# Kernel tuning notes

Hardware: AMD Instinct MI355X
Metric: run time of the kernel (lower is better)

The kernel has to match this reference:

```python
import jax, jax.numpy as jnp
import numpy as np

N = 100_000      # num_nodes
E = 1_600_000    # num_edges (avg degree 16)
D = 64           # embedding_dim
L = 3            # num_layers


def setup_inputs() -> dict:
    key = jax.random.key(0)
    k1, k2 = jax.random.split(key)
    edge_index = jax.random.randint(k1, (2, E), 0, N, dtype=jnp.int64)
    edge_weight = jnp.ones((E,), jnp.float32)
    # nn.init.normal_(std=0.1)
    embedding = 0.1 * jax.random.normal(k2, (N, D), dtype=jnp.float32)
    return {"embedding": embedding, "edge_weight": edge_weight, "edge_index": edge_index}


def reference(embedding, edge_weight, edge_index):
    n = embedding.shape[0]
    self_idx = jnp.arange(n, dtype=edge_index.dtype)
    # add_self_loops: append (i, i) with weight 1 (PyG default fill_value)
    row = jnp.concatenate([edge_index[0], self_idx])  # source j
    col = jnp.concatenate([edge_index[1], self_idx])  # target i
    ew = jnp.concatenate([edge_weight, jnp.ones((n,), embedding.dtype)])
    # degree() counts occurrences of row (unweighted)
    deg = jax.ops.segment_sum(jnp.ones_like(ew), row, num_segments=n)
    deg_inv_sqrt = jnp.where(deg > 0, jax.lax.rsqrt(deg), 0.0)
    norm = deg_inv_sqrt[row] * ew * deg_inv_sqrt[col]  # [E+N]

    x = embedding
    acc = embedding  # running sum of layer-0..L embeddings
    for _ in range(L):
        # gather from source, scale, scatter-add to target (dropout off in eval)
        msg = norm[:, None] * x[row]                       # [E+N, D]
        x = jax.ops.segment_sum(msg, col, num_segments=n)  # [N, D]
        acc = acc + x
    return acc / (L + 1)
```

## Files before the change

kernel.cpp:

```cpp
#include <hip/hip_runtime.h>
#include <stdint.h>

#define DIM 64
#define GB 128
#define GSH 7
#define CH 2048
#define TB1 256
#define BINS2 50000
#define RANGES 2
#define NSLICE 64
#define TBH 1024

__device__ __forceinline__ unsigned bf16rne(float f) {
    unsigned u = __float_as_uint(f);
    return (u + 0x7FFFu + ((u >> 16) & 1u)) >> 16;
}
__device__ __forceinline__ unsigned pack2(float lo, float hi) {
    return bf16rne(lo) | (bf16rne(hi) << 16);
}
#define UNPK(u, lo, hi) { lo = __uint_as_float((u) << 16); hi = __uint_as_float((u) & 0xFFFF0000u); }

__global__ void __launch_bounds__(TBH)
hist_src_kernel(const int* __restrict__ src, const int* __restrict__ dst,
                unsigned short* __restrict__ partials, int* __restrict__ bcnt,
                int E, int N, int Es, int NB) {
    __shared__ unsigned h32[BINS2 / 2];
    __shared__ int hb[1024];
    const int b = blockIdx.x;
    const int r = b / NSLICE, s = b % NSLICE;
    const int base = r * BINS2;
    const int hi = min(base + BINS2, N);
    const int nbw = (hi - base + 1) >> 1;
    for (int j = threadIdx.x; j < nbw; j += TBH) h32[j] = 0;
    if (r == 0) for (int j = threadIdx.x; j < NB; j += TBH) hb[j] = 0;
    __syncthreads();
    const int e0 = s * Es, e1 = min(e0 + Es, E);
    if (r == 0) {
#pragma unroll 4
        for (int i = e0 + threadIdx.x; i < e1; i += TBH) {
            unsigned j = (unsigned)(src[i] - base);
            if (j < (unsigned)BINS2) atomicAdd(&h32[j >> 1], 1u << ((j & 1) * 16));
            atomicAdd(&hb[((unsigned)dst[i]) >> GSH], 1);
        }
    } else {
#pragma unroll 4
        for (int i = e0 + threadIdx.x; i < e1; i += TBH) {
            unsigned j = (unsigned)(src[i] - base);
            if (j < (unsigned)BINS2) atomicAdd(&h32[j >> 1], 1u << ((j & 1) * 16));
        }
    }
    __syncthreads();
    unsigned* part = (unsigned*)(partials + (size_t)s * N + base);
    for (int j = threadIdx.x; j < nbw; j += TBH) part[j] = h32[j];
    if (r == 0)
        for (int j = threadIdx.x; j < NB; j += TBH)
            if (hb[j]) atomicAdd(&bcnt[j], hb[j]);
}

__global__ void __launch_bounds__(256)
merge_dis_kernel(const unsigned short* __restrict__ partials, float* __restrict__ dis, int N) {
    const int i = blockIdx.x * blockDim.x + threadIdx.x;
    if (i >= N) return;
    int od = 0;
    for (int s = 0; s < NSLICE; ++s) od += partials[(size_t)s * N + i];
    dis[i] = rsqrtf((float)od + 1.0f);
}

__global__ void scan_buckets(const int* __restrict__ bcnt, int* __restrict__ bucket_base,
                             int* __restrict__ cursor, int* __restrict__ offsets,
                             int NB, int N) {
    __shared__ int buf[1024];
    const int t = threadIdx.x;
    int v = (t < NB) ? bcnt[t] : 0;
    buf[t] = v;
    __syncthreads();
    for (int off = 1; off < 1024; off <<= 1) {
        int add = (t >= off) ? buf[t - off] : 0;
        __syncthreads();
        buf[t] += add;
        __syncthreads();
    }
    if (t < NB) { bucket_base[t] = buf[t] - v; cursor[t] = buf[t] - v; }
    if (t == NB - 1) { bucket_base[NB] = buf[t]; offsets[N] = buf[t]; }
}

__global__ void __launch_bounds__(TB1)
part_kernel(const int* __restrict__ src, const int* __restrict__ dst,
            const float* __restrict__ ew,
            int* __restrict__ cursor, int2* __restrict__ staged, int E, int NB) {
    __shared__ int h[1024];
    const int tid = threadIdx.x;
    const int e0 = blockIdx.x * CH;
    const int e1 = min(e0 + CH, E);
    for (int j = tid; j < NB; j += TB1) h[j] = 0;
    __syncthreads();
    int4 d[CH / (TB1 * 4)];
    int ngrp = 0;
    for (int i = e0 + tid * 4, k = 0; i < e1; i += TB1 * 4, ++k) {
        int4 t;
        if (i + 3 < e1) t = *(const int4*)(dst + i);
        else {
            t.x = dst[i];
            t.y = (i + 1 < e1) ? dst[i + 1] : -1;
            t.z = (i + 2 < e1) ? dst[i + 2] : -1;
            t.w = (i + 3 < e1) ? dst[i + 3] : -1;
        }
        d[k] = t;
        if (t.x >= 0) atomicAdd(&h[t.x >> GSH], 1);
        if (t.y >= 0) atomicAdd(&h[t.y >> GSH], 1);
        if (t.z >= 0) atomicAdd(&h[t.z >> GSH], 1);
        if (t.w >= 0) atomicAdd(&h[t.w >> GSH], 1);
        ngrp = k + 1;
    }
    __syncthreads();
    for (int j = tid; j < NB; j += TB1) {
        int c = h[j];
        h[j] = c ? atomicAdd(&cursor[j], c) : 0;
    }
    __syncthreads();
    for (int i = e0 + tid * 4, k = 0; k < ngrp; i += TB1 * 4, ++k) {
        int4 t = d[k];
        int4 ss = make_int4(0, 0, 0, 0);
        float4 ww = make_float4(0.f, 0.f, 0.f, 0.f);
        if (i + 3 < e1) { ss = *(const int4*)(src + i); ww = *(const float4*)(ew + i); }
        else {
            ss.x = src[i]; ww.x = ew[i];
            if (i + 1 < e1) { ss.y = src[i + 1]; ww.y = ew[i + 1]; }
            if (i + 2 < e1) { ss.z = src[i + 2]; ww.z = ew[i + 2]; }
            if (i + 3 < e1) { ss.w = src[i + 3]; ww.w = ew[i + 3]; }
        }
#define PART1(T, S, W) if ((T) >= 0) { \
        int pos_ = atomicAdd(&h[(T) >> GSH], 1); \
        staged[pos_] = make_int2((S) | (((T) & (GB - 1)) << 20), __float_as_int(W)); }
        PART1(t.x, ss.x, ww.x)
        PART1(t.y, ss.y, ww.y)
        PART1(t.z, ss.z, ww.z)
        PART1(t.w, ss.w, ww.w)
#undef PART1
    }
}

__global__ void __launch_bounds__(256)
place_kernel(const int2* __restrict__ staged, const int* __restrict__ bucket_base,
             const float* __restrict__ dis,
             int* __restrict__ offsets, int2* __restrict__ csr, int N) {
    __shared__ int cnt[GB];
    __shared__ int cur[GB];
    __shared__ int pre[GB + 1];
    __shared__ float disb[GB];
    const int b = blockIdx.x;
    const int n0 = b << GSH;
    const int nb = min(GB, N - n0);
    const int r0 = bucket_base[b], r1 = bucket_base[b + 1];
    for (int j = threadIdx.x; j < GB; j += 256) cnt[j] = 0;
    for (int j = threadIdx.x; j < nb; j += 256) disb[j] = dis[n0 + j];
    __syncthreads();
    for (int i = r0 + threadIdx.x; i < r1; i += 256)
        atomicAdd(&cnt[(staged[i].x >> 20) & (GB - 1)], 1);
    __syncthreads();
    if (threadIdx.x == 0) {
        int run = r0;
        for (int j = 0; j < nb; ++j) { pre[j] = run; run += cnt[j]; }
        pre[nb] = run;
    }
    __syncthreads();
    for (int j = threadIdx.x; j < nb; j += 256) { offsets[n0 + j] = pre[j]; cur[j] = pre[j]; }
    __syncthreads();
    for (int i = r0 + threadIdx.x; i < r1; i += 256) {
        int2 rec = staged[i];
        int tl = (rec.x >> 20) & (GB - 1);
        int s = rec.x & 0xFFFFF;
        int rank = atomicAdd(&cur[tl], 1);
        float w = dis[s] * __int_as_float(rec.y) * disb[tl];
        csr[rank] = make_int2(s, __float_as_int(w));
    }
}

__global__ void __launch_bounds__(256)
conv_kernel(const float4* __restrict__ in4, uint4* __restrict__ outb, int n8) {
    int i = blockIdx.x * blockDim.x + threadIdx.x;
    if (i >= n8) return;
    float4 a = in4[2 * i], b = in4[2 * i + 1];
    uint4 o;
    o.x = pack2(a.x, a.y); o.y = pack2(a.z, a.w);
    o.z = pack2(b.x, b.y); o.w = pack2(b.z, b.w);
    outb[i] = o;
}

__global__ void __launch_bounds__(256)
prop_kernel(const uint4* __restrict__ xg, const float4* __restrict__ selfF,
            uint4* __restrict__ xstore,
            const int* __restrict__ offsets, const int2* __restrict__ csr,
            const float* __restrict__ dis, int n,
            const float4* __restrict__ embF, const uint4* __restrict__ xaF,
            float4* __restrict__ outF) {
    const int lane = threadIdx.x & 63;
    const int fl  = lane & 7;
    const int sub = lane >> 3;
    const int wave = blockIdx.x * (blockDim.x >> 6) + (threadIdx.x >> 6);
    const int node = wave * 8 + sub;
    if (node >= n) return;

    const int beg = offsets[node];
    const int end = offsets[node + 1];
    const float d = dis[node];
    const float dd = d * d;

    float a0, a1, a2, a3, a4, a5, a6, a7;
    uint4 qs = make_uint4(0, 0, 0, 0);
    if (selfF) {
        float4 s0 = selfF[(size_t)node * 16 + fl * 2];
        float4 s1 = selfF[(size_t)node * 16 + fl * 2 + 1];
        a0 = dd * s0.x; a1 = dd * s0.y; a2 = dd * s0.z; a3 = dd * s0.w;
        a4 = dd * s1.x; a5 = dd * s1.y; a6 = dd * s1.z; a7 = dd * s1.w;
    } else {
        qs = xg[(size_t)node * 8 + fl];
        float l, h;
        UNPK(qs.x, l, h) a0 = dd * l; a1 = dd * h;
        UNPK(qs.y, l, h) a2 = dd * l; a3 = dd * h;
        UNPK(qs.z, l, h) a4 = dd * l; a5 = dd * h;
        UNPK(qs.w, l, h) a6 = dd * l; a7 = dd * h;
    }

#define EDGE(E, Q) { float w_ = __int_as_float((E).y); float l, h; \
    UNPK((Q).x, l, h) a0 = fmaf(w_, l, a0); a1 = fmaf(w_, h, a1); \
    UNPK((Q).y, l, h) a2 = fmaf(w_, l, a2); a3 = fmaf(w_, h, a3); \
    UNPK((Q).z, l, h) a4 = fmaf(w_, l, a4); a5 = fmaf(w_, h, a5); \
    UNPK((Q).w, l, h) a6 = fmaf(w_, l, a6); a7 = fmaf(w_, h, a7); }

    int p = beg;
    for (; p + 8 <= end; p += 8) {
        int2 e0 = csr[p + 0], e1 = csr[p + 1], e2 = csr[p + 2], e3 = csr[p + 3];
        int2 e4 = csr[p + 4], e5 = csr[p + 5], e6 = csr[p + 6], e7 = csr[p + 7];
        uint4 q0 = xg[(size_t)e0.x * 8 + fl];
        uint4 q1 = xg[(size_t)e1.x * 8 + fl];
        uint4 q2 = xg[(size_t)e2.x * 8 + fl];
        uint4 q3 = xg[(size_t)e3.x * 8 + fl];
        uint4 q4 = xg[(size_t)e4.x * 8 + fl];
        uint4 q5 = xg[(size_t)e5.x * 8 + fl];
        uint4 q6 = xg[(size_t)e6.x * 8 + fl];
        uint4 q7 = xg[(size_t)e7.x * 8 + fl];
        EDGE(e0, q0) EDGE(e1, q1) EDGE(e2, q2) EDGE(e3, q3)
        EDGE(e4, q4) EDGE(e5, q5) EDGE(e6, q6) EDGE(e7, q7)
    }
    for (; p + 4 <= end; p += 4) {
        int2 e0 = csr[p + 0], e1 = csr[p + 1], e2 = csr[p + 2], e3 = csr[p + 3];
        uint4 q0 = xg[(size_t)e0.x * 8 + fl];
        uint4 q1 = xg[(size_t)e1.x * 8 + fl];
        uint4 q2 = xg[(size_t)e2.x * 8 + fl];
        uint4 q3 = xg[(size_t)e3.x * 8 + fl];
        EDGE(e0, q0) EDGE(e1, q1) EDGE(e2, q2) EDGE(e3, q3)
    }
    for (; p < end; ++p) {
        int2 e = csr[p];
        uint4 q = xg[(size_t)e.x * 8 + fl];
        EDGE(e, q)
    }
#undef EDGE

    if (outF) {
        float4 eA = embF[(size_t)node * 16 + fl * 2];
        float4 eB = embF[(size_t)node * 16 + fl * 2 + 1];
        uint4 qa = xaF[(size_t)node * 8 + fl];
        float r0 = eA.x + a0, r1 = eA.y + a1, r2 = eA.z + a2, r3 = eA.w + a3;
        float r4 = eB.x + a4, r5 = eB.y + a5, r6 = eB.z + a6, r7 = eB.w + a7;
        float l, h;
        UNPK(qa.x, l, h) r0 += l; r1 += h;
        UNPK(qa.y, l, h) r2 += l; r3 += h;
        UNPK(qa.z, l, h) r4 += l; r5 += h;
        UNPK(qa.w, l, h) r6 += l; r7 += h;
        UNPK(qs.x, l, h) r0 += l; r1 += h;
        UNPK(qs.y, l, h) r2 += l; r3 += h;
        UNPK(qs.z, l, h) r4 += l; r5 += h;
        UNPK(qs.w, l, h) r6 += l; r7 += h;
        outF[(size_t)node * 16 + fl * 2] =
            make_float4(0.25f * r0, 0.25f * r1, 0.25f * r2, 0.25f * r3);
        outF[(size_t)node * 16 + fl * 2 + 1] =
            make_float4(0.25f * r4, 0.25f * r5, 0.25f * r6, 0.25f * r7);
    } else {
        uint4 o;
        o.x = pack2(a0, a1); o.y = pack2(a2, a3);
        o.z = pack2(a4, a5); o.w = pack2(a6, a7);
        xstore[(size_t)node * 8 + fl] = o;
    }
}


extern "C" void kernel_launch(void* const* d_in, const int* in_sizes, int n_in,
                              void* d_out, int out_size, void* d_ws, size_t ws_size,
                              hipStream_t stream) {
    const float* emb = (const float*)d_in[0];
    const float* ew  = (const float*)d_in[1];
    const int*   ei  = (const int*)d_in[2];
    const int E = in_sizes[2] / 2;
    const int N = in_sizes[0] / DIM;
    const int* src = ei;
    const int* dst = ei + E;
    float* out = (float*)d_out;

    const int NB = (N + GB - 1) >> GSH;
    const int Es = (E + NSLICE - 1) / NSLICE;

    char* w = (char*)d_ws;
    size_t xSz = ((size_t)N * DIM * 2 + 255) & ~(size_t)255;
    size_t sSz = ((size_t)E * 8 + 255) & ~(size_t)255;
    size_t pSz = ((size_t)NSLICE * N * 2 + 255) & ~(size_t)255;
    size_t uSz = xSz > sSz ? xSz : sSz; if (pSz > uSz) uSz = pSz;
    unsigned short* partials = (unsigned short*)w;
    int2* staged = (int2*)w;
    uint4* xb    = (uint4*)w; w += uSz;
    int2* csr    = (int2*)w; w += sSz;
    uint4* x0c   = (uint4*)w; w += xSz;
    uint4* xa    = (uint4*)w; w += xSz;
    int* offsets = (int*)w; w += ((size_t)(N + 1) * 4 + 255) & ~(size_t)255;
    float* dis   = (float*)w; w += ((size_t)N * 4 + 255) & ~(size_t)255;
    int* bcnt        = (int*)w; w += 1024 * 4;
    int* bucket_base = (int*)w; w += 1025 * 4;
    int* cursor      = (int*)w; w += 1024 * 4;

    const int TB = 256;
    hipMemsetAsync(bcnt, 0, (size_t)NB * 4, stream);

    hist_src_kernel<<<RANGES * NSLICE, TBH, 0, stream>>>(src, dst, partials, bcnt,
                                                         E, N, Es, NB);
    merge_dis_kernel<<<(N + TB - 1) / TB, TB, 0, stream>>>(partials, dis, N);
    scan_buckets<<<1, 1024, 0, stream>>>(bcnt, bucket_base, cursor, offsets, NB, N);
    part_kernel<<<(E + CH - 1) / CH, TB1, 0, stream>>>(src, dst, ew, cursor,
                                                       staged, E, NB);
    place_kernel<<<NB, TB, 0, stream>>>(staged, bucket_base, dis, offsets, csr, N);

    const int n8 = N * DIM / 8;
    conv_kernel<<<(n8 + TB - 1) / TB, TB, 0, stream>>>((const float4*)emb, x0c, n8);

    dim3 grid((N + 31) / 32), block(TB);
    prop_kernel<<<grid, block, 0, stream>>>(x0c, (const float4*)emb, xa,
                                            offsets, csr, dis, N,
                                            nullptr, nullptr, nullptr);
    prop_kernel<<<grid, block, 0, stream>>>(xa, nullptr, xb,
                                            offsets, csr, dis, N,
                                            nullptr, nullptr, nullptr);
    prop_kernel<<<grid, block, 0, stream>>>(xb, nullptr, nullptr,
                                            offsets, csr, dis, N,
                                            (const float4*)emb, xa, (float4*)out);
}
```

Baseline: 284.0 us.

## Restructure CSR build: 8-bit full-range histograms, fused merge/scan and part/conv

```diff
diff --git a/kernel.cpp b/kernel.cpp
--- a/kernel.cpp
+++ b/kernel.cpp
@@ -2,13 +2,12 @@
 #include <stdint.h>
 
 #define DIM 64
-#define GB 128
-#define GSH 7
+#define GB 256
+#define GSH 8
 #define CH 2048
 #define TB1 256
-#define BINS2 50000
-#define RANGES 2
-#define NSLICE 64
+#define HW 25000
+#define NSL 256
 #define TBH 1024
 
 __device__ __forceinline__ unsigned bf16rne(float f) {
@@ -21,78 +20,96 @@
 #define UNPK(u, lo, hi) { lo = __uint_as_float((u) << 16); hi = __uint_as_float((u) & 0xFFFF0000u); }
 
 __global__ void __launch_bounds__(TBH)
-hist_src_kernel(const int* __restrict__ src, const int* __restrict__ dst,
-                unsigned short* __restrict__ partials, int* __restrict__ bcnt,
-                int E, int N, int Es, int NB) {
-    __shared__ unsigned h32[BINS2 / 2];
-    __shared__ int hb[1024];
-    const int b = blockIdx.x;
-    const int r = b / NSLICE, s = b % NSLICE;
-    const int base = r * BINS2;
-    const int hi = min(base + BINS2, N);
-    const int nbw = (hi - base + 1) >> 1;
-    for (int j = threadIdx.x; j < nbw; j += TBH) h32[j] = 0;
-    if (r == 0) for (int j = threadIdx.x; j < NB; j += TBH) hb[j] = 0;
+hist_kernel(const int* __restrict__ src, const int* __restrict__ dst,
+            unsigned* __restrict__ partials, int* __restrict__ bslice,
+            int E, int N, int Es, int NB) {
+    __shared__ unsigned h8[HW];
+    __shared__ int hb[512];
+    const int s = blockIdx.x;
+    const int nw = (N + 3) >> 2;
+    for (int j = threadIdx.x; j < nw; j += TBH) h8[j] = 0;
+    for (int j = threadIdx.x; j < 512; j += TBH) hb[j] = 0;
     __syncthreads();
     const int e0 = s * Es, e1 = min(e0 + Es, E);
-    if (r == 0) {
 #pragma unroll 4
-        for (int i = e0 + threadIdx.x; i < e1; i += TBH) {
-            unsigned j = (unsigned)(src[i] - base);
-            if (j < (unsigned)BINS2) atomicAdd(&h32[j >> 1], 1u << ((j & 1) * 16));
-            atomicAdd(&hb[((unsigned)dst[i]) >> GSH], 1);
+    for (int i = e0 + threadIdx.x; i < e1; i += TBH) {
+        unsigned sj = (unsigned)src[i];
+        unsigned tj = (unsigned)dst[i];
+        atomicAdd(&h8[sj >> 2], 1u << ((sj & 3) * 8));
+        atomicAdd(&hb[tj >> GSH], 1);
+    }
+    __syncthreads();
+    unsigned* part = partials + (size_t)s * nw;
+    for (int j = threadIdx.x; j < nw; j += TBH) part[j] = h8[j];
+    for (int j = threadIdx.x; j < NB; j += TBH) bslice[s * 512 + j] = hb[j];
+}
+
+__global__ void __launch_bounds__(512)
+merge_scan_kernel(const unsigned* __restrict__ partials, const int* __restrict__ bslice,
+                  float* __restrict__ dis, int* __restrict__ bucket_base,
+                  int* __restrict__ cursor, int* __restrict__ offsets,
+                  int nw, int nmerge, int N, int NB) {
+    __shared__ int buf[512];
+    if ((int)blockIdx.x < nmerge) {
+        const int w = blockIdx.x * 512 + threadIdx.x;
+        if (w >= nw) return;
+        int s0 = 0, s1 = 0, s2 = 0, s3 = 0;
+#pragma unroll 8
+        for (int s = 0; s < NSL; ++s) {
+            unsigned v = partials[(size_t)s * nw + w];
+            s0 += v & 255u; s1 += (v >> 8) & 255u;
+            s2 += (v >> 16) & 255u; s3 += v >> 24;
+        }
+        const int nidx = w * 4;
+        if (nidx + 3 < N) {
+            *(float4*)(dis + nidx) = make_float4(
+                rsqrtf((float)s0 + 1.f), rsqrtf((float)s1 + 1.f),
+                rsqrtf((float)s2 + 1.f), rsqrtf((float)s3 + 1.f));
+        } else {
+            if (nidx + 0 < N) dis[nidx + 0] = rsqrtf((float)s0 + 1.f);
+            if (nidx + 1 < N) dis[nidx + 1] = rsqrtf((float)s1 + 1.f);
+            if (nidx + 2 < N) dis[nidx + 2] = rsqrtf((float)s2 + 1.f);
+            if (nidx + 3 < N) dis[nidx + 3] = rsqrtf((float)s3 + 1.f);
         }
     } else {
-#pragma unroll 4
-        for (int i = e0 + threadIdx.x; i < e1; i += TBH) {
-            unsigned j = (unsigned)(src[i] - base);
-            if (j < (unsigned)BINS2) atomicAdd(&h32[j >> 1], 1u << ((j & 1) * 16));
-        }
-    }
-    __syncthreads();
-    unsigned* part = (unsigned*)(partials + (size_t)s * N + base);
-    for (int j = threadIdx.x; j < nbw; j += TBH) part[j] = h32[j];
-    if (r == 0)
-        for (int j = threadIdx.x; j < NB; j += TBH)
-            if (hb[j]) atomicAdd(&bcnt[j], hb[j]);
-}
-
-__global__ void __launch_bounds__(256)
-merge_dis_kernel(const unsigned short* __restrict__ partials, float* __restrict__ dis, int N) {
-    const int i = blockIdx.x * blockDim.x + threadIdx.x;
-    if (i >= N) return;
-    int od = 0;
-    for (int s = 0; s < NSLICE; ++s) od += partials[(size_t)s * N + i];
-    dis[i] = rsqrtf((float)od + 1.0f);
-}
-
-__global__ void scan_buckets(const int* __restrict__ bcnt, int* __restrict__ bucket_base,
-                             int* __restrict__ cursor, int* __restrict__ offsets,
-                             int NB, int N) {
-    __shared__ int buf[1024];
-    const int t = threadIdx.x;
-    int v = (t < NB) ? bcnt[t] : 0;
-    buf[t] = v;
-    __syncthreads();
-    for (int off = 1; off < 1024; off <<= 1) {
-        int add = (t >= off) ? buf[t - off] : 0;
+        const int t = threadIdx.x;
+        int v = 0;
+        if (t < NB)
+            for (int s = 0; s < NSL; ++s) v += bslice[s * 512 + t];
+        buf[t] = v;
         __syncthreads();
-        buf[t] += add;
-        __syncthreads();
-    }
-    if (t < NB) { bucket_base[t] = buf[t] - v; cursor[t] = buf[t] - v; }
-    if (t == NB - 1) { bucket_base[NB] = buf[t]; offsets[N] = buf[t]; }
+        for (int off = 1; off < 512; off <<= 1) {
+            int add = (t >= off) ? buf[t - off] : 0;
+            __syncthreads();
+            buf[t] += add;
+            __syncthreads();
+        }
+        if (t < NB) { bucket_base[t] = buf[t] - v; cursor[t] = buf[t] - v; }
+        if (t == NB - 1) { bucket_base[NB] = buf[t]; offsets[N] = buf[t]; }
+    }
 }
 
 __global__ void __launch_bounds__(TB1)
-part_kernel(const int* __restrict__ src, const int* __restrict__ dst,
-            const float* __restrict__ ew,
-            int* __restrict__ cursor, int2* __restrict__ staged, int E, int NB) {
-    __shared__ int h[1024];
+part_conv_kernel(const int* __restrict__ src, const int* __restrict__ dst,
+                 const float* __restrict__ ew,
+                 int* __restrict__ cursor, int2* __restrict__ staged,
+                 const float4* __restrict__ emb4, uint4* __restrict__ x0c,
+                 int E, int NB, int npart, int n8) {
+    __shared__ int h[512];
+    if ((int)blockIdx.x >= npart) {
+        const int i = (blockIdx.x - npart) * TB1 + threadIdx.x;
+        if (i >= n8) return;
+        float4 a = emb4[2 * i], b = emb4[2 * i + 1];
+        uint4 o;
+        o.x = pack2(a.x, a.y); o.y = pack2(a.z, a.w);
+        o.z = pack2(b.x, b.y); o.w = pack2(b.z, b.w);
+        x0c[i] = o;
+        return;
+    }
     const int tid = threadIdx.x;
     const int e0 = blockIdx.x * CH;
     const int e1 = min(e0 + CH, E);
-    for (int j = tid; j < NB; j += TB1) h[j] = 0;
+    for (int j = tid; j < 512; j += TB1) h[j] = 0;
     __syncthreads();
     int4 d[CH / (TB1 * 4)];
     int ngrp = 0;
@@ -152,8 +169,8 @@
     const int n0 = b << GSH;
     const int nb = min(GB, N - n0);
     const int r0 = bucket_base[b], r1 = bucket_base[b + 1];
-    for (int j = threadIdx.x; j < GB; j += 256) cnt[j] = 0;
-    for (int j = threadIdx.x; j < nb; j += 256) disb[j] = dis[n0 + j];
+    cnt[threadIdx.x] = 0;
+    disb[threadIdx.x] = (threadIdx.x < nb) ? dis[n0 + threadIdx.x] : 0.f;
     __syncthreads();
     for (int i = r0 + threadIdx.x; i < r1; i += 256)
         atomicAdd(&cnt[(staged[i].x >> 20) & (GB - 1)], 1);
@@ -164,7 +181,7 @@
         pre[nb] = run;
     }
     __syncthreads();
-    for (int j = threadIdx.x; j < nb; j += 256) { offsets[n0 + j] = pre[j]; cur[j] = pre[j]; }
+    if (threadIdx.x < nb) { offsets[n0 + threadIdx.x] = pre[threadIdx.x]; cur[threadIdx.x] = pre[threadIdx.x]; }
     __syncthreads();
     for (int i = r0 + threadIdx.x; i < r1; i += 256) {
         int2 rec = staged[i];
@@ -174,17 +191,6 @@
         float w = dis[s] * __int_as_float(rec.y) * disb[tl];
         csr[rank] = make_int2(s, __float_as_int(w));
     }
-}
-
-__global__ void __launch_bounds__(256)
-conv_kernel(const float4* __restrict__ in4, uint4* __restrict__ outb, int n8) {
-    int i = blockIdx.x * blockDim.x + threadIdx.x;
-    if (i >= n8) return;
-    float4 a = in4[2 * i], b = in4[2 * i + 1];
-    uint4 o;
-    o.x = pack2(a.x, a.y); o.y = pack2(a.z, a.w);
-    o.z = pack2(b.x, b.y); o.w = pack2(b.z, b.w);
-    outb[i] = o;
 }
 
 __global__ void __launch_bounds__(256)
@@ -299,14 +305,15 @@
     float* out = (float*)d_out;
 
     const int NB = (N + GB - 1) >> GSH;
-    const int Es = (E + NSLICE - 1) / NSLICE;
+    const int Es = (E + NSL - 1) / NSL;
+    const int nw = (N + 3) >> 2;
 
     char* w = (char*)d_ws;
     size_t xSz = ((size_t)N * DIM * 2 + 255) & ~(size_t)255;
     size_t sSz = ((size_t)E * 8 + 255) & ~(size_t)255;
-    size_t pSz = ((size_t)NSLICE * N * 2 + 255) & ~(size_t)255;
+    size_t pSz = ((size_t)NSL * nw * 4 + 255) & ~(size_t)255;
     size_t uSz = xSz > sSz ? xSz : sSz; if (pSz > uSz) uSz = pSz;
-    unsigned short* partials = (unsigned short*)w;
+    unsigned* partials = (unsigned*)w;
     int2* staged = (int2*)w;
     uint4* xb    = (uint4*)w; w += uSz;
     int2* csr    = (int2*)w; w += sSz;
@@ -314,23 +321,26 @@
     uint4* xa    = (uint4*)w; w += xSz;
     int* offsets = (int*)w; w += ((size_t)(N + 1) * 4 + 255) & ~(size_t)255;
     float* dis   = (float*)w; w += ((size_t)N * 4 + 255) & ~(size_t)255;
-    int* bcnt        = (int*)w; w += 1024 * 4;
-    int* bucket_base = (int*)w; w += 1025 * 4;
-    int* cursor      = (int*)w; w += 1024 * 4;
+    int* bslice      = (int*)w; w += (size_t)NSL * 512 * 4;
+    int* bucket_base = (int*)w; w += 513 * 4;
+    int* cursor      = (int*)w; w += 512 * 4;
 
     const int TB = 256;
-    hipMemsetAsync(bcnt, 0, (size_t)NB * 4, stream);
-
-    hist_src_kernel<<<RANGES * NSLICE, TBH, 0, stream>>>(src, dst, partials, bcnt,
-                                                         E, N, Es, NB);
-    merge_dis_kernel<<<(N + TB - 1) / TB, TB, 0, stream>>>(partials, dis, N);
-    scan_buckets<<<1, 1024, 0, stream>>>(bcnt, bucket_base, cursor, offsets, NB, N);
-    part_kernel<<<(E + CH - 1) / CH, TB1, 0, stream>>>(src, dst, ew, cursor,
-                                                       staged, E, NB);
+
+    hist_kernel<<<NSL, TBH, 0, stream>>>(src, dst, partials, bslice, E, N, Es, NB);
+
+    const int nmerge = (nw + 511) / 512;
+    merge_scan_kernel<<<nmerge + 1, 512, 0, stream>>>(partials, bslice, dis,
+                                                      bucket_base, cursor, offsets,
+                                                      nw, nmerge, N, NB);
+
+    const int n8 = N * DIM / 8;
+    const int npart = (E + CH - 1) / CH;
+    const int nconv = (n8 + TB - 1) / TB;
+    part_conv_kernel<<<npart + nconv, TB1, 0, stream>>>(src, dst, ew, cursor, staged,
+                                                        (const float4*)emb, x0c,
+                                                        E, NB, npart, n8);
     place_kernel<<<NB, TB, 0, stream>>>(staged, bucket_base, dis, offsets, csr, N);
-
-    const int n8 = N * DIM / 8;
-    conv_kernel<<<(n8 + TB - 1) / TB, TB, 0, stream>>>((const float4*)emb, x0c, n8);
 
     dim3 grid((N + 31) / 32), block(TB);
     prop_kernel<<<grid, block, 0, stream>>>(x0c, (const float4*)emb, xa,
```

New measurement: 274.9 us. -3.2%, faster.
